# Kernel tuning notes

Measured on AMD Instinct MI355X. Metric: run time of the kernel, lower is better.

## Reference

```python
import jax, jax.numpy as jnp
import numpy as np

B = 16384   # batch
F = 26      # categorical fields
N = 100000  # rows per embedding table
M = 16      # embedding dim per field
NUM = 13    # numerical (dense) features
D = F * M + NUM  # embed_output_dim = 429
L = 6       # CrossNet layers (vector parameterization)
H = 1024    # MLP hidden


def setup_inputs() -> dict:
    key = jax.random.key(0)
    ks = jax.random.split(key, 10)
    Xi = jax.random.randint(ks[0], (B, F, 1), 0, N)
    Xv = jax.random.normal(ks[1], (B, NUM), dtype=jnp.float32)
    # per-field tables, init U(-sqrt(1/n), sqrt(1/n)) as in the torch code; stacked flat
    bound = float(np.sqrt(1.0 / N))
    emb_tables = jax.random.uniform(ks[2], (F * N, M), jnp.float32, -bound, bound)
    cross_w = jax.random.normal(ks[3], (L, D), dtype=jnp.float32) * 0.02
    cross_b = jnp.zeros((L, D), dtype=jnp.float32)
    W1 = jax.random.normal(ks[4], (D, H), dtype=jnp.float32) * (1.0 / np.sqrt(D))
    b1 = jnp.zeros((H,), dtype=jnp.float32)
    W2 = jax.random.normal(ks[5], (H, H), dtype=jnp.float32) * (1.0 / np.sqrt(H))
    b2 = jnp.zeros((H,), dtype=jnp.float32)
    Wout = jax.random.normal(ks[6], (H + D, 1), dtype=jnp.float32) * (1.0 / np.sqrt(H + D))
    bout = jnp.zeros((1,), dtype=jnp.float32)
    return dict(Xi=Xi, Xv=Xv, emb_tables=emb_tables, cross_w=cross_w,
                cross_b=cross_b, W1=W1, b1=b1, W2=W2, b2=b2, Wout=Wout, bout=bout)


def reference(Xi, Xv, emb_tables, cross_w, cross_b, W1, b1, W2, b2, Wout, bout):
    # Fused multi-table EmbeddingBag(mode='sum'): one gather over the stacked tables.
    offs = (jnp.arange(F, dtype=Xi.dtype) * N)[None, :, None]        # [1,F,1]
    flat_idx = (Xi + offs).reshape(-1)                               # [B*F*K]
    g = emb_tables[flat_idx].reshape(B, F, -1, M).sum(axis=2)        # [B,F,M] bag-sum
    x0 = jnp.concatenate([Xv, g.reshape(B, F * M)], axis=1)          # [B,D]
    # CrossNet, vector parameterization: x_{l+1} = x0 * (x_l . w_l) + b_l + x_l
    x = x0
    for l in range(L):
        xw = x @ cross_w[l]                                          # [B]
        x = x0 * xw[:, None] + cross_b[l] + x
    # Deep MLP on x0
    h = jax.nn.relu(x0 @ W1 + b1)
    h = jax.nn.relu(h @ W2 + b2)
    out = jnp.concatenate([h, x], axis=1) @ Wout + bout              # [B,1]
    return out[:, 0]
```

## Files before the change

### kernel.cpp

```cpp
#include <hip/hip_runtime.h>
#include <hip/hip_bf16.h>

#define B_   16384
#define F_   26
#define N_   100000
#define M_   16
#define NUM_ 13
#define D_   429
#define KP1_ 448
#define L_   6
#define H_   1024

typedef unsigned short u16;
typedef __bf16 bf16x8 __attribute__((ext_vector_type(8)));
typedef float  f32x4  __attribute__((ext_vector_type(4)));

__device__ __forceinline__ u16 f2bf_bits(float f) {
  union { float f; unsigned u; } x; x.f = f;
  unsigned r = x.u + 0x7FFFu + ((x.u >> 16) & 1u);
  return (u16)(r >> 16);
}

__global__ __launch_bounds__(256) void fused_front(
    const int* __restrict__ Xi, const float* __restrict__ Xv,
    const float* __restrict__ emb,
    const float* __restrict__ cw, const float* __restrict__ cb,
    const float* __restrict__ Wout, const float* __restrict__ bout,
    const float* __restrict__ W1, const float* __restrict__ W2,
    u16* __restrict__ x0b, u16* __restrict__ w1bt, u16* __restrict__ w2bt,
    float* __restrict__ out) {
  __shared__ u16 sbuf[4][KP1_];
  const int blk = blockIdx.x;
  if (blk < B_ / 4) {
    const int w = threadIdx.x >> 6, lane = threadIdx.x & 63;
    const int b = blk * 4 + w;
    const int* xi = Xi + b * F_;

    float x0r[7];
    #pragma unroll
    for (int i = 0; i < 7; ++i) {
      int e = i * 64 + lane;
      float v = 0.f;
      if (e < 416) {
        int f = e >> 4;
        int idx = xi[f];
        v = emb[((size_t)f * N_ + idx) * M_ + (e & 15)];
      } else if (e < D_) {
        v = Xv[b * NUM_ + (e - 416)];
      }
      x0r[i] = v;
      sbuf[w][e] = f2bf_bits(v);
    }

    float xr[7];
    #pragma unroll
    for (int i = 0; i < 7; ++i) xr[i] = x0r[i];
    for (int l = 0; l < L_; ++l) {
      float wl[7], bl[7];
      #pragma unroll
      for (int i = 0; i < 7; ++i) {
        int e = i * 64 + lane;
        if (e < D_) {
          int d = (e < 416) ? (13 + e) : (e - 416);
          wl[i] = cw[l * D_ + d]; bl[i] = cb[l * D_ + d];
        } else { wl[i] = 0.f; bl[i] = 0.f; }
      }
      float s = 0.f;
      #pragma unroll
      for (int i = 0; i < 7; ++i) s += xr[i] * wl[i];
      #pragma unroll
      for (int off = 32; off; off >>= 1) s += __shfl_xor(s, off);
      #pragma unroll
      for (int i = 0; i < 7; ++i) xr[i] = x0r[i] * s + bl[i] + xr[i];
    }

    __syncthreads();
    if (lane < 56)
      ((uint4*)(x0b + (size_t)b * KP1_))[lane] = ((const uint4*)sbuf[w])[lane];

    float s = 0.f;
    #pragma unroll
    for (int i = 0; i < 7; ++i) {
      int e = i * 64 + lane;
      if (e < D_) {
        int d = (e < 416) ? (13 + e) : (e - 416);
        s += xr[i] * Wout[H_ + d];
      }
    }
    #pragma unroll
    for (int off = 32; off; off >>= 1) s += __shfl_xor(s, off);
    if (lane == 0) out[b] = s + bout[0];
  } else {
    int t = (blk - B_ / 4) * 256 + threadIdx.x;
    if (t < H_ * KP1_) {
      int n = t / KP1_, e = t % KP1_;
      float v = 0.f;
      if (e < D_) {
        int d = (e < 416) ? (13 + e) : (e - 416);
        v = W1[(size_t)d * H_ + n];
      }
      w1bt[t] = f2bf_bits(v);
    } else {
      int t2 = t - H_ * KP1_;
      if (t2 < H_ * H_) {
        int n = t2 / H_, k = t2 % H_;
        w2bt[t2] = f2bf_bits(W2[(size_t)k * H_ + n]);
      }
    }
  }
}

template<int MODE>
__global__ __launch_bounds__(512, 2) void gemm256(
    const u16* __restrict__ A, const u16* __restrict__ BT,
    const float* __restrict__ bias, u16* __restrict__ C,
    const float* __restrict__ Wout, float* __restrict__ out,
    int N, int K) {
  __shared__ __align__(16) u16 As[4][256 * 32];
  __shared__ __align__(16) u16 Bs[4][256 * 32];
  const int nbx = N >> 8;
  const int cpx = gridDim.x >> 3;
  const int swz = (blockIdx.x & 7) * cpx + (blockIdx.x >> 3);
  const int bx = swz % nbx;
  const int by = swz / nbx;
  const int tid = threadIdx.x;
  const int w = tid >> 6, l = tid & 63;
  const int wr = w >> 2, wc = w & 3;
  const int nkt = K >> 5;

  const int srow = l >> 2;
  const int schunk = (l & 3) ^ ((l >> 3) & 3);
  const u16* gA = A  + (size_t)(by * 256 + w * 16 + srow) * K + schunk * 8;
  const u16* gB = BT + (size_t)(bx * 256 + w * 16 + srow) * K + schunk * 8;
  const int ldsoff = w * 16 * 32;

  auto stage = [&](int t) {
    const int buf = t & 3;
    const u16* a = gA + t * 32;
    const u16* b = gB + t * 32;
    #pragma unroll
    for (int i = 0; i < 2; ++i)
      __builtin_amdgcn_global_load_lds(
          (const __attribute__((address_space(1))) void*)(a + (size_t)i * 128 * K),
          (__attribute__((address_space(3))) void*)&As[buf][ldsoff + i * 128 * 32], 16, 0, 0);
    #pragma unroll
    for (int i = 0; i < 2; ++i)
      __builtin_amdgcn_global_load_lds(
          (const __attribute__((address_space(1))) void*)(b + (size_t)i * 128 * K),
          (__attribute__((address_space(3))) void*)&Bs[buf][ldsoff + i * 128 * 32], 16, 0, 0);
  };

  const int fr = l & 15;
  const int fs = ((l >> 4) ^ ((fr >> 1) & 3)) << 4;
  const int aoff = (wr * 128 + fr) * 64 + fs;
  const int boff = (wc * 64 + fr) * 64 + fs;

  auto read_frags = [&](int tt, bf16x8 (&af)[8], bf16x8 (&bf)[4]) {
    const char* Ab = (const char*)&As[tt & 3][0];
    const char* Bb = (const char*)&Bs[tt & 3][0];
    #pragma unroll
    for (int m = 0; m < 8; ++m) af[m] = *(const bf16x8*)(Ab + aoff + m * 1024);
    #pragma unroll
    for (int n = 0; n < 4; ++n) bf[n] = *(const bf16x8*)(Bb + boff + n * 1024);
  };

  f32x4 acc[8][4] = {};
  auto mfma_all = [&](bf16x8 (&af)[8], bf16x8 (&bf)[4]) {
    __builtin_amdgcn_s_setprio(1);
    #pragma unroll
    for (int m = 0; m < 8; ++m)
      #pragma unroll
      for (int n = 0; n < 4; ++n)
        acc[m][n] = __builtin_amdgcn_mfma_f32_16x16x32_bf16(af[m], bf[n], acc[m][n], 0, 0, 0);
    __builtin_amdgcn_s_setprio(0);
  };

  stage(0); stage(1); stage(2);
  asm volatile("s_waitcnt vmcnt(4)" ::: "memory");
  __builtin_amdgcn_s_barrier();
  bf16x8 afA[8], bfA[4], afB[8], bfB[4];
  read_frags(0, afA, bfA);

  for (int t = 0; t < nkt; t += 2) {
    if (t + 3 < nkt) stage(t + 3);
    if (t + 1 < nkt) read_frags(t + 1, afB, bfB);
    mfma_all(afA, bfA);
    if (t + 2 < nkt) {
      if (t + 3 < nkt) asm volatile("s_waitcnt vmcnt(4)" ::: "memory");
      else             asm volatile("s_waitcnt vmcnt(0)" ::: "memory");
      __builtin_amdgcn_s_barrier();
    }
    const int u = t + 1;
    if (u < nkt) {
      if (u + 3 < nkt) stage(u + 3);
      if (u + 1 < nkt) read_frags(u + 1, afA, bfA);
      mfma_all(afB, bfB);
      if (u + 2 < nkt) {
        if (u + 3 < nkt) asm volatile("s_waitcnt vmcnt(4)" ::: "memory");
        else             asm volatile("s_waitcnt vmcnt(0)" ::: "memory");
        __builtin_amdgcn_s_barrier();
      }
    }
  }

  const int g4 = l >> 4;
  const int ccol0 = bx * 256 + wc * 64;
  const int row0 = by * 256 + wr * 128 + g4 * 4;
  if (MODE == 0) {
    #pragma unroll
    for (int n = 0; n < 4; ++n) {
      int col = ccol0 + n * 16 + fr;
      float bv = bias[col];
      #pragma unroll
      for (int m = 0; m < 8; ++m)
        #pragma unroll
        for (int r = 0; r < 4; ++r) {
          float v = fmaxf(acc[m][n][r] + bv, 0.f);
          C[(size_t)(row0 + m * 16 + r) * N + col] = f2bf_bits(v);
        }
    }
  } else {
    float bv[4], wv[4];
    #pragma unroll
    for (int n = 0; n < 4; ++n) {
      int col = ccol0 + n * 16 + fr;
      bv[n] = bias[col]; wv[n] = Wout[col];
    }
    #pragma unroll
    for (int m = 0; m < 8; ++m)
      #pragma unroll
      for (int r = 0; r < 4; ++r) {
        float s = 0.f;
        #pragma unroll
        for (int n = 0; n < 4; ++n) {
          float v = fmaxf(acc[m][n][r] + bv[n], 0.f);
          s = fmaf(v, wv[n], s);
        }
        s += __shfl_xor(s, 1); s += __shfl_xor(s, 2);
        s += __shfl_xor(s, 4); s += __shfl_xor(s, 8);
        if (fr == 0) atomicAdd(out + row0 + m * 16 + r, s);
      }
  }
}

extern "C" void kernel_launch(void* const* d_in, const int* in_sizes, int n_in,
                              void* d_out, int out_size, void* d_ws, size_t ws_size,
                              hipStream_t stream) {
  const int*   Xi   = (const int*)d_in[0];
  const float* Xv   = (const float*)d_in[1];
  const float* emb  = (const float*)d_in[2];
  const float* cw   = (const float*)d_in[3];
  const float* cb   = (const float*)d_in[4];
  const float* W1   = (const float*)d_in[5];
  const float* b1   = (const float*)d_in[6];
  const float* W2   = (const float*)d_in[7];
  const float* b2   = (const float*)d_in[8];
  const float* Wout = (const float*)d_in[9];
  const float* bout = (const float*)d_in[10];
  float* out = (float*)d_out;

  char* ws = (char*)d_ws;
  size_t off = 0;
  auto alloc = [&](size_t bytes) {
    void* p = ws + off; off += (bytes + 255) & ~(size_t)255; return p;
  };
  u16* x0b  = (u16*)alloc((size_t)B_ * KP1_ * 2);
  u16* w1bt = (u16*)alloc((size_t)H_ * KP1_ * 2);
  u16* w2bt = (u16*)alloc((size_t)H_ * H_ * 2);
  u16* h1   = (u16*)alloc((size_t)B_ * H_ * 2);

  const int prep_blocks = (H_ * KP1_ + H_ * H_) / 256;
  hipLaunchKernelGGL(fused_front, dim3(B_ / 4 + prep_blocks), dim3(256), 0, stream,
                     Xi, Xv, emb, cw, cb, Wout, bout, W1, W2, x0b, w1bt, w2bt, out);
  hipLaunchKernelGGL((gemm256<0>), dim3((B_ / 256) * (H_ / 256)), dim3(512), 0, stream,
                     x0b, w1bt, b1, h1, nullptr, nullptr, H_, KP1_);
  hipLaunchKernelGGL((gemm256<1>), dim3((B_ / 256) * (H_ / 256)), dim3(512), 0, stream,
                     h1, w2bt, b2, nullptr, Wout, out, H_, H_);
}
```

Before: 107.2 us.

## Restructure GEMM main loop to BK=64 double-buffer with split A/B staging

Rewrites the bf16 MFMA GEMM mainloop from a 4-stage BK=32 ring buffer to a 2-stage BK=64 double buffer. Each K tile is processed in four sub-phases of 16 MFMAs, with loads of the next A and B tiles interleaved between phases and fenced by sched_barriers and workgroup barriers. The LDS layout and XOR swizzle are changed to match 128-byte rows. This cuts fragment register pressure and makes the load/compute interleave explicit, in exchange for more barriers per tile and a shallower prefetch depth that may expose global latency.

```diff
diff --git a/kernel.cpp b/kernel.cpp
--- a/kernel.cpp
+++ b/kernel.cpp
@@ -116,96 +116,124 @@
     const float* __restrict__ bias, u16* __restrict__ C,
     const float* __restrict__ Wout, float* __restrict__ out,
     int N, int K) {
-  __shared__ __align__(16) u16 As[4][256 * 32];
-  __shared__ __align__(16) u16 Bs[4][256 * 32];
+  __shared__ __align__(16) u16 As[2][256 * 64];
+  __shared__ __align__(16) u16 Bs[2][256 * 64];
   const int nbx = N >> 8;
   const int cpx = gridDim.x >> 3;
   const int swz = (blockIdx.x & 7) * cpx + (blockIdx.x >> 3);
   const int bx = swz % nbx;
   const int by = swz / nbx;
   const int tid = threadIdx.x;
-  const int w = tid >> 6, l = tid & 63;
+  const int l = tid & 63;
+  const int w = tid >> 6;
   const int wr = w >> 2, wc = w & 3;
-  const int nkt = K >> 5;
-
-  const int srow = l >> 2;
-  const int schunk = (l & 3) ^ ((l >> 3) & 3);
-  const u16* gA = A  + (size_t)(by * 256 + w * 16 + srow) * K + schunk * 8;
-  const u16* gB = BT + (size_t)(bx * 256 + w * 16 + srow) * K + schunk * 8;
-  const int ldsoff = w * 16 * 32;
-
-  auto stage = [&](int t) {
-    const int buf = t & 3;
-    const u16* a = gA + t * 32;
-    const u16* b = gB + t * 32;
-    #pragma unroll
-    for (int i = 0; i < 2; ++i)
+  const int nkt = K >> 6;
+
+  const int r0 = tid >> 3;
+  const int scol = ((tid & 7) ^ (r0 & 7)) << 4;
+  const char* gA = (const char*)(A + (size_t)(by * 256 + r0) * K) + scol;
+  const char* gB = (const char*)(BT + (size_t)(bx * 256 + r0) * K) + scol;
+  const size_t rowstep = (size_t)64 * K * 2;
+  const int dst0 = tid * 8;
+
+  auto stageA = [&](int t) {
+    const int buf = t & 1;
+    const char* src = gA + (size_t)t * 128;
+    #pragma unroll
+    for (int i = 0; i < 4; ++i)
       __builtin_amdgcn_global_load_lds(
-          (const __attribute__((address_space(1))) void*)(a + (size_t)i * 128 * K),
-          (__attribute__((address_space(3))) void*)&As[buf][ldsoff + i * 128 * 32], 16, 0, 0);
-    #pragma unroll
-    for (int i = 0; i < 2; ++i)
+          (const __attribute__((address_space(1))) void*)(src + i * rowstep),
+          (__attribute__((address_space(3))) void*)&As[buf][dst0 + i * 4096], 16, 0, 0);
+  };
+  auto stageB = [&](int t) {
+    const int buf = t & 1;
+    const char* src = gB + (size_t)t * 128;
+    #pragma unroll
+    for (int i = 0; i < 4; ++i)
       __builtin_amdgcn_global_load_lds(
-          (const __attribute__((address_space(1))) void*)(b + (size_t)i * 128 * K),
-          (__attribute__((address_space(3))) void*)&Bs[buf][ldsoff + i * 128 * 32], 16, 0, 0);
+          (const __attribute__((address_space(1))) void*)(src + i * rowstep),
+          (__attribute__((address_space(3))) void*)&Bs[buf][dst0 + i * 4096], 16, 0, 0);
   };
 
-  const int fr = l & 15;
-  const int fs = ((l >> 4) ^ ((fr >> 1) & 3)) << 4;
-  const int aoff = (wr * 128 + fr) * 64 + fs;
-  const int boff = (wc * 64 + fr) * 64 + fs;
-
-  auto read_frags = [&](int tt, bf16x8 (&af)[8], bf16x8 (&bf)[4]) {
-    const char* Ab = (const char*)&As[tt & 3][0];
-    const char* Bb = (const char*)&Bs[tt & 3][0];
-    #pragma unroll
-    for (int m = 0; m < 8; ++m) af[m] = *(const bf16x8*)(Ab + aoff + m * 1024);
-    #pragma unroll
-    for (int n = 0; n < 4; ++n) bf[n] = *(const bf16x8*)(Bb + boff + n * 1024);
-  };
+  const int fr = l & 15, g = l >> 4;
+  const int csw = (g * 16) ^ ((fr & 7) << 4);
+  const int aoff = (wr * 128 + fr) * 128 + csw;
+  const int boff = (wc * 64 + fr) * 128 + csw;
 
   f32x4 acc[8][4] = {};
-  auto mfma_all = [&](bf16x8 (&af)[8], bf16x8 (&bf)[4]) {
+
+  stageA(0); stageB(0);
+  asm volatile("s_waitcnt vmcnt(0)" ::: "memory");
+  __builtin_amdgcn_s_barrier();
+
+  for (int t = 0; t < nkt; ++t) {
+    const char* Ab = (const char*)&As[t & 1][0];
+    const char* Bb = (const char*)&Bs[t & 1][0];
+    const bool pre = (t + 1 < nkt);
+    bf16x8 af[4], bf[4];
+
+    #pragma unroll
+    for (int m = 0; m < 4; ++m) af[m] = *(const bf16x8*)(Ab + aoff + m * 2048);
+    #pragma unroll
+    for (int n = 0; n < 4; ++n) bf[n] = *(const bf16x8*)(Bb + boff + n * 2048);
+    if (pre) stageA(t + 1);
+    __builtin_amdgcn_sched_barrier(0);
+    __builtin_amdgcn_s_barrier();
     __builtin_amdgcn_s_setprio(1);
     #pragma unroll
-    for (int m = 0; m < 8; ++m)
+    for (int m = 0; m < 4; ++m)
       #pragma unroll
       for (int n = 0; n < 4; ++n)
         acc[m][n] = __builtin_amdgcn_mfma_f32_16x16x32_bf16(af[m], bf[n], acc[m][n], 0, 0, 0);
     __builtin_amdgcn_s_setprio(0);
-  };
-
-  stage(0); stage(1); stage(2);
-  asm volatile("s_waitcnt vmcnt(4)" ::: "memory");
-  __builtin_amdgcn_s_barrier();
-  bf16x8 afA[8], bfA[4], afB[8], bfB[4];
-  read_frags(0, afA, bfA);
-
-  for (int t = 0; t < nkt; t += 2) {
-    if (t + 3 < nkt) stage(t + 3);
-    if (t + 1 < nkt) read_frags(t + 1, afB, bfB);
-    mfma_all(afA, bfA);
-    if (t + 2 < nkt) {
-      if (t + 3 < nkt) asm volatile("s_waitcnt vmcnt(4)" ::: "memory");
-      else             asm volatile("s_waitcnt vmcnt(0)" ::: "memory");
-      __builtin_amdgcn_s_barrier();
-    }
-    const int u = t + 1;
-    if (u < nkt) {
-      if (u + 3 < nkt) stage(u + 3);
-      if (u + 1 < nkt) read_frags(u + 1, afA, bfA);
-      mfma_all(afB, bfB);
-      if (u + 2 < nkt) {
-        if (u + 3 < nkt) asm volatile("s_waitcnt vmcnt(4)" ::: "memory");
-        else             asm volatile("s_waitcnt vmcnt(0)" ::: "memory");
-        __builtin_amdgcn_s_barrier();
-      }
-    }
+    __builtin_amdgcn_s_barrier();
+
+    #pragma unroll
+    for (int m = 0; m < 4; ++m) af[m] = *(const bf16x8*)(Ab + aoff + (m + 4) * 2048);
+    if (pre) stageB(t + 1);
+    __builtin_amdgcn_sched_barrier(0);
+    __builtin_amdgcn_s_barrier();
+    __builtin_amdgcn_s_setprio(1);
+    #pragma unroll
+    for (int m = 0; m < 4; ++m)
+      #pragma unroll
+      for (int n = 0; n < 4; ++n)
+        acc[m + 4][n] = __builtin_amdgcn_mfma_f32_16x16x32_bf16(af[m], bf[n], acc[m + 4][n], 0, 0, 0);
+    __builtin_amdgcn_s_setprio(0);
+    __builtin_amdgcn_s_barrier();
+
+    #pragma unroll
+    for (int m = 0; m < 4; ++m) af[m] = *(const bf16x8*)(Ab + (aoff ^ 64) + m * 2048);
+    #pragma unroll
+    for (int n = 0; n < 4; ++n) bf[n] = *(const bf16x8*)(Bb + (boff ^ 64) + n * 2048);
+    __builtin_amdgcn_sched_barrier(0);
+    __builtin_amdgcn_s_barrier();
+    __builtin_amdgcn_s_setprio(1);
+    #pragma unroll
+    for (int m = 0; m < 4; ++m)
+      #pragma unroll
+      for (int n = 0; n < 4; ++n)
+        acc[m][n] = __builtin_amdgcn_mfma_f32_16x16x32_bf16(af[m], bf[n], acc[m][n], 0, 0, 0);
+    __builtin_amdgcn_s_setprio(0);
+    __builtin_amdgcn_s_barrier();
+
+    #pragma unroll
+    for (int m = 0; m < 4; ++m) af[m] = *(const bf16x8*)(Ab + (aoff ^ 64) + (m + 4) * 2048);
+    __builtin_amdgcn_sched_barrier(0);
+    __builtin_amdgcn_s_barrier();
+    __builtin_amdgcn_s_setprio(1);
+    #pragma unroll
+    for (int m = 0; m < 4; ++m)
+      #pragma unroll
+      for (int n = 0; n < 4; ++n)
+        acc[m + 4][n] = __builtin_amdgcn_mfma_f32_16x16x32_bf16(af[m], bf[n], acc[m + 4][n], 0, 0, 0);
+    __builtin_amdgcn_s_setprio(0);
+    if (pre) asm volatile("s_waitcnt vmcnt(0)" ::: "memory");
+    __builtin_amdgcn_s_barrier();
   }
 
-  const int g4 = l >> 4;
   const int ccol0 = bx * 256 + wc * 64;
-  const int row0 = by * 256 + wr * 128 + g4 * 4;
+  const int row0 = by * 256 + wr * 128 + g * 4;
   if (MODE == 0) {
     #pragma unroll
     for (int n = 0; n < 4; ++n) {
```

Measured after the change: 98.81 us. 7.9% less time.

## Restructure GEMM main loop into ping-pong schedule and tile weight transposes

Applied to the files above, without the earlier changes.

The GEMM K loop is rewritten to stage 64-wide K chunks in two double-buffered halves. Each wave computes its 128-row tile as two 64-row accumulator halves, with barrier-separated MFMA phases interleaved with LDS fragment reads and async global-to-LDS loads. This is meant to overlap memory and MFMA more tightly and lower fragment register pressure. The first-layer K padding grows from 448 to 512 so K divides into 128-wide iterations, at the cost of extra zero work. The weight transpose/convert prep now goes through 64x64 LDS tiles with vectorized reads and writes, replacing scalar strided accesses.

```diff
diff --git a/kernel.cpp b/kernel.cpp
--- a/kernel.cpp
+++ b/kernel.cpp
@@ -7,7 +7,7 @@
 #define M_   16
 #define NUM_ 13
 #define D_   429
-#define KP1_ 448
+#define KP1_ 512
 #define L_   6
 #define H_   1024
 
@@ -29,10 +29,12 @@
     const float* __restrict__ W1, const float* __restrict__ W2,
     u16* __restrict__ x0b, u16* __restrict__ w1bt, u16* __restrict__ w2bt,
     float* __restrict__ out) {
-  __shared__ u16 sbuf[4][KP1_];
+  __shared__ __align__(16) u16 sbuf[4][KP1_];
+  __shared__ __align__(16) float tile[64][68];
   const int blk = blockIdx.x;
+  const int tid = threadIdx.x;
   if (blk < B_ / 4) {
-    const int w = threadIdx.x >> 6, lane = threadIdx.x & 63;
+    const int w = tid >> 6, lane = tid & 63;
     const int b = blk * 4 + w;
     const int* xi = Xi + b * F_;
 
@@ -51,6 +53,7 @@
       x0r[i] = v;
       sbuf[w][e] = f2bf_bits(v);
     }
+    sbuf[w][448 + lane] = 0;
 
     float xr[7];
     #pragma unroll
@@ -75,8 +78,7 @@
     }
 
     __syncthreads();
-    if (lane < 56)
-      ((uint4*)(x0b + (size_t)b * KP1_))[lane] = ((const uint4*)sbuf[w])[lane];
+    ((uint4*)(x0b + (size_t)b * KP1_))[lane] = ((const uint4*)sbuf[w])[lane];
 
     float s = 0.f;
     #pragma unroll
@@ -91,24 +93,63 @@
     for (int off = 32; off; off >>= 1) s += __shfl_xor(s, off);
     if (lane == 0) out[b] = s + bout[0];
   } else {
-    int t = (blk - B_ / 4) * 256 + threadIdx.x;
-    if (t < H_ * KP1_) {
-      int n = t / KP1_, e = t % KP1_;
-      float v = 0.f;
-      if (e < D_) {
-        int d = (e < 416) ? (13 + e) : (e - 416);
-        v = W1[(size_t)d * H_ + n];
-      }
-      w1bt[t] = f2bf_bits(v);
+    int pid = blk - B_ / 4;
+    if (pid < 112) {
+      const int ti = pid >> 4, tj = pid & 15;
+      const int e0 = ti * 64, c0 = tj * 64;
+      #pragma unroll
+      for (int it = 0; it < 4; ++it) {
+        int el = it * 16 + (tid >> 4);
+        int e = e0 + el;
+        int d = (e < 416) ? (13 + e) : ((e < D_) ? (e - 416) : -1);
+        float4 v = make_float4(0.f, 0.f, 0.f, 0.f);
+        if (d >= 0) v = *(const float4*)&W1[(size_t)d * H_ + c0 + (tid & 15) * 4];
+        *(float4*)&tile[el][(tid & 15) * 4] = v;
+      }
+      __syncthreads();
+      const int nl = tid >> 2, ks = (tid & 3) * 16;
+      u16 tmp[16];
+      #pragma unroll
+      for (int x = 0; x < 16; ++x) tmp[x] = f2bf_bits(tile[ks + x][nl]);
+      uint4* dst = (uint4*)&w1bt[(size_t)(c0 + nl) * KP1_ + e0 + ks];
+      dst[0] = *(uint4*)&tmp[0];
+      dst[1] = *(uint4*)&tmp[8];
     } else {
-      int t2 = t - H_ * KP1_;
-      if (t2 < H_ * H_) {
-        int n = t2 / H_, k = t2 % H_;
-        w2bt[t2] = f2bf_bits(W2[(size_t)k * H_ + n]);
-      }
+      pid -= 112;
+      const int ti = pid >> 4, tj = pid & 15;
+      const int k0 = ti * 64, c0 = tj * 64;
+      #pragma unroll
+      for (int it = 0; it < 4; ++it) {
+        int kl = it * 16 + (tid >> 4);
+        *(float4*)&tile[kl][(tid & 15) * 4] =
+            *(const float4*)&W2[(size_t)(k0 + kl) * H_ + c0 + (tid & 15) * 4];
+      }
+      __syncthreads();
+      const int nl = tid >> 2, ks = (tid & 3) * 16;
+      u16 tmp[16];
+      #pragma unroll
+      for (int x = 0; x < 16; ++x) tmp[x] = f2bf_bits(tile[ks + x][nl]);
+      uint4* dst = (uint4*)&w2bt[(size_t)(c0 + nl) * H_ + k0 + ks];
+      dst[0] = *(uint4*)&tmp[0];
+      dst[1] = *(uint4*)&tmp[8];
     }
   }
 }
+
+#define BARR __builtin_amdgcn_s_barrier()
+#define SBR  __builtin_amdgcn_sched_barrier(0)
+#define VM6  asm volatile("s_waitcnt vmcnt(6)" ::: "memory")
+#define VM0  asm volatile("s_waitcnt vmcnt(0)" ::: "memory")
+#define MM(ACC) do { \
+  __builtin_amdgcn_s_setprio(1); \
+  _Pragma("unroll") \
+  for (int mi = 0; mi < 4; ++mi) { \
+    _Pragma("unroll") \
+    for (int ni = 0; ni < 4; ++ni) \
+      ACC[mi][ni] = __builtin_amdgcn_mfma_f32_16x16x32_bf16(af[mi], bfc[ni], ACC[mi][ni], 0, 0, 0); \
+  } \
+  __builtin_amdgcn_s_setprio(0); \
+} while (0)
 
 template<int MODE>
 __global__ __launch_bounds__(512, 2) void gemm256(
@@ -116,107 +157,118 @@
     const float* __restrict__ bias, u16* __restrict__ C,
     const float* __restrict__ Wout, float* __restrict__ out,
     int N, int K) {
-  __shared__ __align__(16) u16 As[4][256 * 32];
-  __shared__ __align__(16) u16 Bs[4][256 * 32];
+  __shared__ __align__(16) u16 As[2][2][256 * 32];
+  __shared__ __align__(16) u16 Bs[2][2][256 * 32];
   const int nbx = N >> 8;
   const int cpx = gridDim.x >> 3;
   const int swz = (blockIdx.x & 7) * cpx + (blockIdx.x >> 3);
   const int bx = swz % nbx;
   const int by = swz / nbx;
   const int tid = threadIdx.x;
-  const int w = tid >> 6, l = tid & 63;
+  const int l = tid & 63;
+  const int w = tid >> 6;
   const int wr = w >> 2, wc = w & 3;
-  const int nkt = K >> 5;
-
-  const int srow = l >> 2;
-  const int schunk = (l & 3) ^ ((l >> 3) & 3);
-  const u16* gA = A  + (size_t)(by * 256 + w * 16 + srow) * K + schunk * 8;
-  const u16* gB = BT + (size_t)(bx * 256 + w * 16 + srow) * K + schunk * 8;
-  const int ldsoff = w * 16 * 32;
-
-  auto stage = [&](int t) {
-    const int buf = t & 3;
-    const u16* a = gA + t * 32;
-    const u16* b = gB + t * 32;
-    #pragma unroll
-    for (int i = 0; i < 2; ++i)
-      __builtin_amdgcn_global_load_lds(
-          (const __attribute__((address_space(1))) void*)(a + (size_t)i * 128 * K),
-          (__attribute__((address_space(3))) void*)&As[buf][ldsoff + i * 128 * 32], 16, 0, 0);
-    #pragma unroll
-    for (int i = 0; i < 2; ++i)
-      __builtin_amdgcn_global_load_lds(
-          (const __attribute__((address_space(1))) void*)(b + (size_t)i * 128 * K),
-          (__attribute__((address_space(3))) void*)&Bs[buf][ldsoff + i * 128 * 32], 16, 0, 0);
-  };
-
-  const int fr = l & 15;
-  const int fs = ((l >> 4) ^ ((fr >> 1) & 3)) << 4;
-  const int aoff = (wr * 128 + fr) * 64 + fs;
-  const int boff = (wc * 64 + fr) * 64 + fs;
-
-  auto read_frags = [&](int tt, bf16x8 (&af)[8], bf16x8 (&bf)[4]) {
-    const char* Ab = (const char*)&As[tt & 3][0];
-    const char* Bb = (const char*)&Bs[tt & 3][0];
-    #pragma unroll
-    for (int m = 0; m < 8; ++m) af[m] = *(const bf16x8*)(Ab + aoff + m * 1024);
-    #pragma unroll
-    for (int n = 0; n < 4; ++n) bf[n] = *(const bf16x8*)(Bb + boff + n * 1024);
-  };
-
-  f32x4 acc[8][4] = {};
-  auto mfma_all = [&](bf16x8 (&af)[8], bf16x8 (&bf)[4]) {
-    __builtin_amdgcn_s_setprio(1);
-    #pragma unroll
-    for (int m = 0; m < 8; ++m)
-      #pragma unroll
-      for (int n = 0; n < 4; ++n)
-        acc[m][n] = __builtin_amdgcn_mfma_f32_16x16x32_bf16(af[m], bf[n], acc[m][n], 0, 0, 0);
-    __builtin_amdgcn_s_setprio(0);
-  };
-
-  stage(0); stage(1); stage(2);
-  asm volatile("s_waitcnt vmcnt(4)" ::: "memory");
-  __builtin_amdgcn_s_barrier();
-  bf16x8 afA[8], bfA[4], afB[8], bfB[4];
-  read_frags(0, afA, bfA);
-
-  for (int t = 0; t < nkt; t += 2) {
-    if (t + 3 < nkt) stage(t + 3);
-    if (t + 1 < nkt) read_frags(t + 1, afB, bfB);
-    mfma_all(afA, bfA);
-    if (t + 2 < nkt) {
-      if (t + 3 < nkt) asm volatile("s_waitcnt vmcnt(4)" ::: "memory");
-      else             asm volatile("s_waitcnt vmcnt(0)" ::: "memory");
-      __builtin_amdgcn_s_barrier();
-    }
-    const int u = t + 1;
-    if (u < nkt) {
-      if (u + 3 < nkt) stage(u + 3);
-      if (u + 1 < nkt) read_frags(u + 1, afA, bfA);
-      mfma_all(afB, bfB);
-      if (u + 2 < nkt) {
-        if (u + 3 < nkt) asm volatile("s_waitcnt vmcnt(4)" ::: "memory");
-        else             asm volatile("s_waitcnt vmcnt(0)" ::: "memory");
-        __builtin_amdgcn_s_barrier();
-      }
-    }
+  const int niter = K >> 7;
+
+  const int sr = tid >> 2;
+  const int scs = ((tid & 3) ^ ((tid >> 3) & 3)) * 8;
+  const u16* gA0 = A  + (size_t)(by * 256 + sr) * K + scs;
+  const u16* gB0 = BT + (size_t)(bx * 256 + sr) * K + scs;
+  const int dst0 = tid * 8;
+
+  auto stgA = [&](int t, int kk) {
+    const u16* s = gA0 + t * 64 + kk * 32;
+    __builtin_amdgcn_global_load_lds(
+        (const __attribute__((address_space(1))) void*)s,
+        (__attribute__((address_space(3))) void*)&As[t & 1][kk][dst0], 16, 0, 0);
+    __builtin_amdgcn_global_load_lds(
+        (const __attribute__((address_space(1))) void*)(s + (size_t)128 * K),
+        (__attribute__((address_space(3))) void*)&As[t & 1][kk][dst0 + 4096], 16, 0, 0);
+  };
+  auto stgB = [&](int t, int kk) {
+    const u16* s = gB0 + t * 64 + kk * 32;
+    __builtin_amdgcn_global_load_lds(
+        (const __attribute__((address_space(1))) void*)s,
+        (__attribute__((address_space(3))) void*)&Bs[t & 1][kk][dst0], 16, 0, 0);
+    __builtin_amdgcn_global_load_lds(
+        (const __attribute__((address_space(1))) void*)(s + (size_t)128 * K),
+        (__attribute__((address_space(3))) void*)&Bs[t & 1][kk][dst0 + 4096], 16, 0, 0);
+  };
+
+  const int fr = l & 15, g = l >> 4;
+  const int slot = (g ^ ((fr >> 1) & 3)) * 16;
+  const int aoff = (wr * 128 + fr) * 64 + slot;
+  const int boff = (wc * 64 + fr) * 64 + slot;
+
+  bf16x8 af[4], bfc[4];
+  auto rdA = [&](int buf, int kk, int mlo) {
+    const char* base = (const char*)&As[buf][kk][0];
+    #pragma unroll
+    for (int m = 0; m < 4; ++m)
+      af[m] = *(const bf16x8*)(base + aoff + (mlo + m) * 1024);
+  };
+  auto rdB = [&](int buf, int kk) {
+    const char* base = (const char*)&Bs[buf][kk][0];
+    #pragma unroll
+    for (int n = 0; n < 4; ++n)
+      bfc[n] = *(const bf16x8*)(base + boff + n * 1024);
+  };
+
+  f32x4 accLo[4][4] = {};
+  f32x4 accHi[4][4] = {};
+
+  stgA(0, 0); stgB(0, 0); stgA(0, 1); stgB(0, 1);
+  stgB(1, 0); stgA(1, 0); stgB(1, 1);
+  VM6;
+  BARR;
+
+  for (int j = 0; j < niter; ++j) {
+    const int t1 = 2 * j + 1;
+    const bool stg = (j + 1 < niter);
+    rdA(0, 0, 0); rdB(0, 0);
+    stgA(t1, 1);
+    SBR; BARR; MM(accLo); BARR;
+    rdA(0, 0, 4);
+    if (stg) stgB(t1 + 1, 0);
+    SBR; BARR; MM(accHi); BARR;
+    rdA(0, 1, 0); rdB(0, 1);
+    if (stg) stgA(t1 + 1, 0);
+    SBR; BARR; MM(accLo); BARR;
+    rdA(0, 1, 4);
+    if (stg) stgB(t1 + 1, 1);
+    SBR; BARR; MM(accHi);
+    if (stg) { VM6; } else { VM0; }
+    BARR;
+    rdA(1, 0, 0); rdB(1, 0);
+    if (stg) stgA(t1 + 1, 1);
+    SBR; BARR; MM(accLo); BARR;
+    rdA(1, 0, 4);
+    if (stg) stgB(t1 + 2, 0);
+    SBR; BARR; MM(accHi); BARR;
+    rdA(1, 1, 0); rdB(1, 1);
+    if (stg) stgA(t1 + 2, 0);
+    SBR; BARR; MM(accLo); BARR;
+    rdA(1, 1, 4);
+    if (stg) stgB(t1 + 2, 1);
+    SBR; BARR; MM(accHi);
+    if (stg) { VM6; BARR; }
   }
 
-  const int g4 = l >> 4;
   const int ccol0 = bx * 256 + wc * 64;
-  const int row0 = by * 256 + wr * 128 + g4 * 4;
+  const int row0 = by * 256 + wr * 128 + g * 4;
   if (MODE == 0) {
     #pragma unroll
     for (int n = 0; n < 4; ++n) {
       int col = ccol0 + n * 16 + fr;
       float bv = bias[col];
       #pragma unroll
-      for (int m = 0; m < 8; ++m)
+      for (int m = 0; m < 4; ++m)
         #pragma unroll
         for (int r = 0; r < 4; ++r) {
-          float v = fmaxf(acc[m][n][r] + bv, 0.f);
-          C[(size_t)(row0 + m * 16 + r) * N + col] = f2bf_bits(v);
+          float v0 = fmaxf(accLo[m][n][r] + bv, 0.f);
+          C[(size_t)(row0 + m * 16 + r) * N + col] = f2bf_bits(v0);
+          float v1 = fmaxf(accHi[m][n][r] + bv, 0.f);
+          C[(size_t)(row0 + 64 + m * 16 + r) * N + col] = f2bf_bits(v1);
         }
     }
   } else {
@@ -227,18 +279,23 @@
       bv[n] = bias[col]; wv[n] = Wout[col];
     }
     #pragma unroll
-    for (int m = 0; m < 8; ++m)
+    for (int m = 0; m < 4; ++m)
       #pragma unroll
       for (int r = 0; r < 4; ++r) {
-        float s = 0.f;
+        float s0 = 0.f, s1 = 0.f;
         #pragma unroll
         for (int n = 0; n < 4; ++n) {
-          float v = fmaxf(acc[m][n][r] + bv[n], 0.f);
-          s = fmaf(v, wv[n], s);
+          s0 = fmaf(fmaxf(accLo[m][n][r] + bv[n], 0.f), wv[n], s0);
+          s1 = fmaf(fmaxf(accHi[m][n][r] + bv[n], 0.f), wv[n], s1);
         }
-        s += __shfl_xor(s, 1); s += __shfl_xor(s, 2);
-        s += __shfl_xor(s, 4); s += __shfl_xor(s, 8);
-        if (fr == 0) atomicAdd(out + row0 + m * 16 + r, s);
+        s0 += __shfl_xor(s0, 1); s0 += __shfl_xor(s0, 2);
+        s0 += __shfl_xor(s0, 4); s0 += __shfl_xor(s0, 8);
+        s1 += __shfl_xor(s1, 1); s1 += __shfl_xor(s1, 2);
+        s1 += __shfl_xor(s1, 4); s1 += __shfl_xor(s1, 8);
+        if (fr == 0) {
+          atomicAdd(out + row0 + m * 16 + r, s0);
+          atomicAdd(out + row0 + 64 + m * 16 + r, s1);
+        }
       }
   }
 }
@@ -269,8 +326,7 @@
   u16* w2bt = (u16*)alloc((size_t)H_ * H_ * 2);
   u16* h1   = (u16*)alloc((size_t)B_ * H_ * 2);
 
-  const int prep_blocks = (H_ * KP1_ + H_ * H_) / 256;
-  hipLaunchKernelGGL(fused_front, dim3(B_ / 4 + prep_blocks), dim3(256), 0, stream,
+  hipLaunchKernelGGL(fused_front, dim3(B_ / 4 + 112 + 256), dim3(256), 0, stream,
                      Xi, Xv, emb, cw, cb, Wout, bout, W1, W2, x0b, w1bt, w2bt, out);
   hipLaunchKernelGGL((gemm256<0>), dim3((B_ / 256) * (H_ / 256)), dim3(512), 0, stream,
                      x0b, w1bt, b1, h1, nullptr, nullptr, H_, KP1_);
```

New measurement: 94.63 us. -11.8%, faster.
